# Performance work log

Measured on AMD Instinct MI355X. Metric: run time of the kernel, lower is better.

Reference implementation:

```python
import jax, jax.numpy as jnp
import numpy as np

B, C, H, W = 2, 512, 128, 128
L_NUM, HEADS, LEVELS, POINTS = 6, 8, 1, 4
HEAD_DIM = C // HEADS


def setup_inputs() -> dict:
    key = jax.random.key(0)
    ks = jax.random.split(key, 16)
    s = 0.02
    rn = lambda k, shape, scale=s: jax.random.normal(k, shape, jnp.float32) * scale
    return dict(
        bev_feat=jax.random.normal(ks[0], (B, C, H, W), jnp.float32),
        lidar_feat=jax.random.normal(ks[1], (B, C, H, W), jnp.float32),
        Wv=rn(ks[2], (L_NUM, C, C)), bv=jnp.zeros((L_NUM, C), jnp.float32),
        Woff=rn(ks[3], (L_NUM, C, HEADS * LEVELS * POINTS * 2)),
        boff=rn(ks[4], (L_NUM, HEADS * LEVELS * POINTS * 2), 0.5),
        Waw=rn(ks[5], (L_NUM, C, HEADS * LEVELS * POINTS)),
        baw=jnp.zeros((L_NUM, HEADS * LEVELS * POINTS), jnp.float32),
        Wout=rn(ks[6], (L_NUM, C, C)), bout=jnp.zeros((L_NUM, C), jnp.float32),
        ln1_g=jnp.ones((L_NUM, C), jnp.float32), ln1_b=jnp.zeros((L_NUM, C), jnp.float32),
        W1=rn(ks[7], (L_NUM, C, C)), W2=rn(ks[8], (L_NUM, C, C)),
        ln2_g=jnp.ones((L_NUM, C), jnp.float32), ln2_b=jnp.zeros((L_NUM, C), jnp.float32),
        pe_W1=rn(ks[9], (2, C), 0.5),
        pe_bn_g=jnp.ones((C,), jnp.float32), pe_bn_b=jnp.zeros((C,), jnp.float32),
        pe_bn_m=jnp.zeros((C,), jnp.float32), pe_bn_v=jnp.ones((C,), jnp.float32),
        pe_W2=rn(ks[10], (C, C)),
    )


def _layer_norm(x, g, b):
    mu = jnp.mean(x, -1, keepdims=True)
    var = jnp.mean((x - mu) ** 2, -1, keepdims=True)
    return (x - mu) * jax.lax.rsqrt(var + 1e-5) * g + b


def _bilinear_gather(v_flat, locx, locy):
    # v_flat: (B, heads, H*W, d); locx/locy: (B, heads, S) normalized [0,1]
    # grid_sample semantics: align_corners=False, zero padding
    x = locx * W - 0.5
    y = locy * H - 0.5
    x0f = jnp.floor(x); y0f = jnp.floor(y)
    wx = x - x0f; wy = y - y0f
    x0 = x0f.astype(jnp.int32); y0 = y0f.astype(jnp.int32)

    def corner(xi, yi, w):
        inb = (xi >= 0) & (xi < W) & (yi >= 0) & (yi < H)
        idx = jnp.clip(yi, 0, H - 1) * W + jnp.clip(xi, 0, W - 1)
        g = jnp.take_along_axis(v_flat, idx[..., None], axis=2)
        return g * (w * inb)[..., None]

    return (corner(x0, y0, (1 - wx) * (1 - wy)) + corner(x0 + 1, y0, wx * (1 - wy))
            + corner(x0, y0 + 1, (1 - wx) * wy) + corner(x0 + 1, y0 + 1, wx * wy))


def reference(bev_feat, lidar_feat, Wv, bv, Woff, boff, Waw, baw, Wout, bout,
              ln1_g, ln1_b, W1, W2, ln2_g, ln2_b,
              pe_W1, pe_bn_g, pe_bn_b, pe_bn_m, pe_bn_v, pe_W2):
    N = H * W
    # sparse voxelization: keep rows with all-nonzero features, pack valid-first per batch
    lf = jnp.transpose(lidar_feat, (0, 2, 3, 1)).reshape(B, N, C)
    mask = jnp.all(lf != 0, axis=-1)                       # (B,N)
    order = jnp.argsort((~mask).astype(jnp.int32), axis=1, stable=True)  # valid first
    valid = jnp.take_along_axis(mask, order, axis=1)       # (B,N)
    q = jnp.take_along_axis(lf, order[..., None], axis=1) * valid[..., None]
    hh = jnp.arange(N) // W
    ww = jnp.arange(N) % W
    ref_all = jnp.stack([ww / W, hh / H], -1).astype(jnp.float32)  # (N,2) = (x,y)
    ref = jnp.broadcast_to(ref_all, (B, N, 2))
    ref = jnp.take_along_axis(ref, order[..., None], axis=1) * valid[..., None]
    # learned positional embedding (BatchNorm in eval mode)
    pe = ref.reshape(B * N, 2) @ pe_W1
    pe = (pe - pe_bn_m) * jax.lax.rsqrt(pe_bn_v + 1e-5) * pe_bn_g + pe_bn_b
    q_pos = (jax.nn.relu(pe) @ pe_W2).reshape(B, N, C)
    feat_flat = jnp.transpose(bev_feat.reshape(B, C, N), (0, 2, 1))  # (B,N,C)
    norm_xy = jnp.array([W, H], jnp.float32)  # offset normalizer per level (w,h)
    for i in range(L_NUM):
        ident = q
        x = q + q_pos
        v = (feat_flat @ Wv[i] + bv[i]).reshape(B, N, HEADS, HEAD_DIM)
        v_flat = jnp.transpose(v, (0, 2, 1, 3))  # (B,heads,N,d)
        off = (x @ Woff[i] + boff[i]).reshape(B, N, HEADS, LEVELS * POINTS, 2)
        aw = jax.nn.softmax((x @ Waw[i] + baw[i]).reshape(B, N, HEADS, LEVELS * POINTS), axis=-1)
        loc = ref[:, :, None, None, :] + off / norm_xy      # (B,N,heads,P,2)
        locx = jnp.transpose(loc[..., 0], (0, 2, 1, 3)).reshape(B, HEADS, N * POINTS)
        locy = jnp.transpose(loc[..., 1], (0, 2, 1, 3)).reshape(B, HEADS, N * POINTS)
        samp = _bilinear_gather(v_flat, locx, locy).reshape(B, HEADS, N, POINTS, HEAD_DIM)
        awt = jnp.transpose(aw, (0, 2, 1, 3))               # (B,heads,N,P)
        out = jnp.sum(samp * awt[..., None], axis=3)        # (B,heads,N,d)
        out = jnp.transpose(out, (0, 2, 1, 3)).reshape(B, N, C)
        q = out @ Wout[i] + bout[i] + ident                 # dropout in eval = identity
        q = _layer_norm(q, ln1_g[i], ln1_b[i])
        q = jax.nn.relu(q @ W1[i]) @ W2[i] + q
        q = _layer_norm(q, ln2_g[i], ln2_b[i])
    # scatter back to dense (B,C,H,W); invalid voxels stay zero
    slots = jnp.zeros((B, N, C), q.dtype)
    slots = slots.at[jnp.arange(B)[:, None], order].set(q * valid[..., None])
    return jnp.transpose(slots.reshape(B, H, W, C), (0, 3, 1, 2))
```

## Files before the change

### kernel.cpp

```cpp
#include <hip/hip_runtime.h>
#include <cstdint>
#include <cstddef>

#define BDIM 2
#define CDIM 512
#define HDIM 128
#define WDIM 128
#define NDIM (HDIM * WDIM)
#define LNUM 6
#define NHEADS 8
#define HEAD_DIM 64
#define NPTS 4
#define BN_TOT (BDIM * NDIM)

typedef unsigned short u16;
typedef __attribute__((ext_vector_type(8))) short bf16x8;
typedef __attribute__((ext_vector_type(4))) float f32x4;

__device__ __forceinline__ u16 f2bf(float x) {
    unsigned u = __float_as_uint(x);
    u += 0x7fffu + ((u >> 16) & 1u);
    return (u16)(u >> 16);
}
__device__ __forceinline__ float bf2f(u16 h) {
    return __uint_as_float(((unsigned)h) << 16);
}

__device__ __forceinline__ void load_lds16(const void* g, void* l) {
    __builtin_amdgcn_global_load_lds(
        (const __attribute__((address_space(1))) void*)g,
        (__attribute__((address_space(3))) void*)l, 16, 0, 0);
}

__global__ void mask_kernel(const float* __restrict__ lidar, int* __restrict__ mask)
{
    int idx = blockIdx.x * blockDim.x + threadIdx.x;
    if (idx >= BN_TOT) return;
    int b = idx / NDIM;
    int n = idx - b * NDIM;
    const float* p = lidar + (size_t)b * CDIM * NDIM + n;
    int ok = 1;
#pragma unroll 8
    for (int c = 0; c < CDIM; ++c)
        ok &= (p[(size_t)c * NDIM] != 0.0f);
    mask[idx] = ok;
}

__global__ void order_kernel(const int* __restrict__ mask, int* __restrict__ order,
                             int* __restrict__ nvalid)
{
    int b = blockIdx.x;
    const int* m = mask + b * NDIM;
    int* ord = order + b * NDIM;
    __shared__ int part[256];
    __shared__ int totalValid;
    int t = threadIdx.x;
    const int CHUNK = NDIM / 256;
    int base = t * CHUNK;
    int cnt = 0;
    for (int i = 0; i < CHUNK; ++i) cnt += m[base + i];
    part[t] = cnt;
    __syncthreads();
    for (int s = 1; s < 256; s <<= 1) {
        int v = (t >= s) ? part[t - s] : 0;
        __syncthreads();
        part[t] += v;
        __syncthreads();
    }
    if (t == 255) { totalValid = part[255]; nvalid[b] = part[255]; }
    __syncthreads();
    int validBefore = (t == 0) ? 0 : part[t - 1];
    int nv = totalValid;
    for (int i = 0; i < CHUNK; ++i) {
        int n = base + i;
        if (m[n]) { ord[validBefore] = n; validBefore++; }
        else      { int invBefore = n - validBefore; ord[nv + invBefore] = n; }
    }
}

__global__ void ref_kernel(const int* __restrict__ order, const int* __restrict__ nvalid,
                           float* __restrict__ ref)
{
    int idx = blockIdx.x * blockDim.x + threadIdx.x;
    if (idx >= BN_TOT) return;
    int b = idx / NDIM;
    int j = idx - b * NDIM;
    int n = order[idx];
    float flag = (j < nvalid[b]) ? 1.0f : 0.0f;
    int hh = n / WDIM;
    int ww = n - hh * WDIM;
    ref[(size_t)idx * 2 + 0] = ((float)ww / (float)WDIM) * flag;
    ref[(size_t)idx * 2 + 1] = ((float)hh / (float)HDIM) * flag;
}

__global__ void pack_q_kernel(const float* __restrict__ lidar, const int* __restrict__ order,
                              const int* __restrict__ nvalid, u16* __restrict__ q)
{
    __shared__ float tile[32][33];
    __shared__ int ord_s[32];
    int b  = blockIdx.z;
    int j0 = blockIdx.x * 32;
    int c0 = blockIdx.y * 32;
    int tx = threadIdx.x, ty = threadIdx.y;
    if (ty == 0) ord_s[tx] = order[b * NDIM + j0 + tx];
    __syncthreads();
    const float* src = lidar + (size_t)b * CDIM * NDIM;
#pragma unroll
    for (int k = 0; k < 4; ++k) {
        int cl = ty * 4 + k;
        tile[cl][tx] = src[(size_t)(c0 + cl) * NDIM + ord_s[tx]];
    }
    __syncthreads();
    int nv = nvalid[b];
#pragma unroll
    for (int k = 0; k < 4; ++k) {
        int jl = ty * 4 + k;
        int j = j0 + jl;
        float f = (j < nv) ? 1.0f : 0.0f;
        q[((size_t)b * NDIM + j) * CDIM + c0 + tx] = f2bf(tile[tx][jl] * f);
    }
}

__global__ void scatter_kernel(const u16* __restrict__ q, const int* __restrict__ order,
                               const int* __restrict__ nvalid, float* __restrict__ out)
{
    __shared__ float tile[32][33];
    __shared__ int ord_s[32];
    int b  = blockIdx.z;
    int j0 = blockIdx.x * 32;
    int c0 = blockIdx.y * 32;
    int tx = threadIdx.x, ty = threadIdx.y;
    if (ty == 0) ord_s[tx] = order[b * NDIM + j0 + tx];
    __syncthreads();
    int nv = nvalid[b];
#pragma unroll
    for (int k = 0; k < 4; ++k) {
        int jl = ty * 4 + k;
        int j = j0 + jl;
        float f = (j < nv) ? 1.0f : 0.0f;
        tile[jl][tx] = bf2f(q[((size_t)b * NDIM + j) * CDIM + c0 + tx]) * f;
    }
    __syncthreads();
    float* dst = out + (size_t)b * CDIM * NDIM;
#pragma unroll
    for (int k = 0; k < 4; ++k) {
        int cl = ty * 4 + k;
        dst[(size_t)(c0 + cl) * NDIM + ord_s[tx]] = tile[tx][cl];
    }
}

__global__ void tconv_b_kernel(const float* __restrict__ src0, u16* __restrict__ dst0)
{
    __shared__ float t[32][33];
    int z = blockIdx.z;
    const float* src = src0 + (size_t)z * 512 * 512;
    u16* dst = dst0 + (size_t)z * 512 * 512;
    int k0 = blockIdx.x * 32, n0 = blockIdx.y * 32;
    int tx = threadIdx.x, ty = threadIdx.y;
#pragma unroll
    for (int j = 0; j < 4; ++j) {
        int kl = ty * 4 + j;
        t[kl][tx] = src[(size_t)(k0 + kl) * 512 + n0 + tx];
    }
    __syncthreads();
#pragma unroll
    for (int j = 0; j < 4; ++j) {
        int nl = ty * 4 + j;
        dst[(size_t)(n0 + nl) * 512 + k0 + tx] = f2bf(t[tx][nl]);
    }
}

__global__ void tconv_offaw_b_kernel(const float* __restrict__ woff0,
                                     const float* __restrict__ waw0,
                                     u16* __restrict__ dst0)
{
    __shared__ float t[32][33];
    int z = blockIdx.z;
    const float* woff = woff0 + (size_t)z * 512 * 64;
    const float* waw  = waw0 + (size_t)z * 512 * 32;
    u16* dst = dst0 + (size_t)z * 96 * 512;
    int k0 = blockIdx.x * 32, n0 = blockIdx.y * 32;
    int tx = threadIdx.x, ty = threadIdx.y;
#pragma unroll
    for (int j = 0; j < 4; ++j) {
        int kl = ty * 4 + j;
        int n = n0 + tx;
        float v = (n < 64) ? woff[(size_t)(k0 + kl) * 64 + n]
                           : waw[(size_t)(k0 + kl) * 32 + (n - 64)];
        t[kl][tx] = v;
    }
    __syncthreads();
#pragma unroll
    for (int j = 0; j < 4; ++j) {
        int nl = ty * 4 + j;
        dst[(size_t)(n0 + nl) * 512 + k0 + tx] = f2bf(t[tx][nl]);
    }
}

__global__ void bev_conv_kernel(const float* __restrict__ bev, u16* __restrict__ dst)
{
    __shared__ float t[32][33];
    int b  = blockIdx.z;
    int n0 = blockIdx.x * 32;
    int c0 = blockIdx.y * 32;
    int tx = threadIdx.x, ty = threadIdx.y;
    const float* src = bev + (size_t)b * CDIM * NDIM;
#pragma unroll
    for (int j = 0; j < 4; ++j) {
        int cl = ty * 4 + j;
        t[cl][tx] = src[(size_t)(c0 + cl) * NDIM + n0 + tx];
    }
    __syncthreads();
#pragma unroll
    for (int j = 0; j < 4; ++j) {
        int nl = ty * 4 + j;
        dst[((size_t)b * NDIM + n0 + nl) * CDIM + c0 + tx] = f2bf(t[tx][nl]);
    }
}

__global__ void pe_hidden_kernel(const float* __restrict__ ref, const float* __restrict__ W1,
                                 const float* __restrict__ g, const float* __restrict__ bb,
                                 const float* __restrict__ m, const float* __restrict__ v,
                                 u16* __restrict__ out)
{
    int row = blockIdx.x;
    float r0 = ref[(size_t)row * 2 + 0];
    float r1 = ref[(size_t)row * 2 + 1];
    for (int c = threadIdx.x; c < CDIM; c += blockDim.x) {
        float pe = r0 * W1[c] + r1 * W1[CDIM + c];
        pe = (pe - m[c]) * rsqrtf(v[c] + 1e-5f) * g[c] + bb[c];
        out[(size_t)row * CDIM + c] = f2bf(fmaxf(pe, 0.0f));
    }
}

__global__ void add_bf_kernel(const u16* __restrict__ q, const u16* __restrict__ qpos,
                              u16* __restrict__ x)
{
    size_t i = (size_t)blockIdx.x * blockDim.x + threadIdx.x;
    uint4 qa = ((const uint4*)q)[i];
    uint4 pv = ((const uint4*)qpos)[i];
    unsigned qw[4] = {qa.x, qa.y, qa.z, qa.w};
    unsigned pw[4] = {pv.x, pv.y, pv.z, pv.w};
    unsigned rw[4];
#pragma unroll
    for (int k = 0; k < 4; ++k) {
        float a0 = bf2f((u16)(qw[k] & 0xffff)), a1 = bf2f((u16)(qw[k] >> 16));
        float p0 = bf2f((u16)(pw[k] & 0xffff)), p1 = bf2f((u16)(pw[k] >> 16));
        rw[k] = (unsigned)f2bf(a0 + p0) | ((unsigned)f2bf(a1 + p1) << 16);
    }
    uint4 r; r.x = rw[0]; r.y = rw[1]; r.z = rw[2]; r.w = rw[3];
    ((uint4*)x)[i] = r;
}

__global__ __launch_bounds__(256) void gemm_bf16(
    const u16* __restrict__ A, const u16* __restrict__ Bt,
    const float* __restrict__ bias, u16* __restrict__ outB, int relu)
{
    __shared__ u16 As[2][128 * 32];
    __shared__ u16 Bs[2][128 * 32];
    int tid = threadIdx.x;
    int wave = tid >> 6, lane = tid & 63;
    int wr = wave >> 1, wc = wave & 1;
    int quad = lane >> 4, l15 = lane & 15;
    int bm = blockIdx.y * 128, bn = blockIdx.x * 128;

    f32x4 acc[4][4];
#pragma unroll
    for (int i = 0; i < 4; ++i)
#pragma unroll
        for (int j = 0; j < 4; ++j) { f32x4 z = {0.f, 0.f, 0.f, 0.f}; acc[i][j] = z; }

    int e0 = wave * 512 + lane * 8;
    int e1 = (wave + 4) * 512 + lane * 8;
    const u16* Ag0 = A + (size_t)(bm + (e0 >> 5)) * 512 + (e0 & 31);
    const u16* Ag1 = A + (size_t)(bm + (e1 >> 5)) * 512 + (e1 & 31);
    const u16* Bg0 = Bt + (size_t)(bn + (e0 >> 5)) * 512 + (e0 & 31);
    const u16* Bg1 = Bt + (size_t)(bn + (e1 >> 5)) * 512 + (e1 & 31);

    load_lds16(Ag0, &As[0][wave * 512]);
    load_lds16(Ag1, &As[0][(wave + 4) * 512]);
    load_lds16(Bg0, &Bs[0][wave * 512]);
    load_lds16(Bg1, &Bs[0][(wave + 4) * 512]);

    for (int it = 0; it < 16; ++it) {
        __syncthreads();
        int cur = it & 1, nxt = cur ^ 1;
        if (it < 15) {
            int kn = (it + 1) * 32;
            load_lds16(Ag0 + kn, &As[nxt][wave * 512]);
            load_lds16(Ag1 + kn, &As[nxt][(wave + 4) * 512]);
            load_lds16(Bg0 + kn, &Bs[nxt][wave * 512]);
            load_lds16(Bg1 + kn, &Bs[nxt][(wave + 4) * 512]);
        }
        bf16x8 av[4], bv[4];
#pragma unroll
        for (int mi = 0; mi < 4; ++mi)
            av[mi] = *(const bf16x8*)&As[cur][(wr * 64 + mi * 16 + l15) * 32 + quad * 8];
#pragma unroll
        for (int ni = 0; ni < 4; ++ni)
            bv[ni] = *(const bf16x8*)&Bs[cur][(wc * 64 + ni * 16 + l15) * 32 + quad * 8];
#pragma unroll
        for (int mi = 0; mi < 4; ++mi)
#pragma unroll
            for (int ni = 0; ni < 4; ++ni)
                acc[mi][ni] = __builtin_amdgcn_mfma_f32_16x16x32_bf16(
                    av[mi], bv[ni], acc[mi][ni], 0, 0, 0);
    }

    int rowb = bm + wr * 64;
    int colb = bn + wc * 64;
#pragma unroll
    for (int mi = 0; mi < 4; ++mi) {
#pragma unroll
        for (int ni = 0; ni < 4; ++ni) {
            int col = colb + ni * 16 + l15;
            float bi = bias ? bias[col] : 0.0f;
#pragma unroll
            for (int r = 0; r < 4; ++r) {
                int row = rowb + mi * 16 + quad * 4 + r;
                float val = acc[mi][ni][r] + bi;
                if (relu) val = fmaxf(val, 0.0f);
                outB[(size_t)row * 512 + col] = f2bf(val);
            }
        }
    }
}

__global__ __launch_bounds__(512, 4) void gemm_ln(
    const u16* __restrict__ A, const u16* __restrict__ Bt,
    const float* __restrict__ bias, const u16* __restrict__ resid,
    const float* __restrict__ g, const float* __restrict__ bta,
    u16* __restrict__ outQ, const u16* __restrict__ qpos, u16* __restrict__ outX)
{
    __shared__ u16 As[2][64 * 32];
    __shared__ u16 Bs[2][512 * 32];
    __shared__ float rs[8][64];
    __shared__ float rq[8][64];
    __shared__ float muL[64], invL[64];

    int tid = threadIdx.x;
    int wv = tid >> 6, lane = tid & 63;
    int quad = lane >> 4, l15 = lane & 15;
    int bm = blockIdx.x * 64;

    f32x4 acc[4][4];
#pragma unroll
    for (int i = 0; i < 4; ++i)
#pragma unroll
        for (int j = 0; j < 4; ++j) { f32x4 z = {0.f, 0.f, 0.f, 0.f}; acc[i][j] = z; }

    const u16* Ag = A + (size_t)(bm + wv * 16 + (lane >> 2)) * 512 + (lane & 3) * 8;
    const u16* Bg[4];
#pragma unroll
    for (int it = 0; it < 4; ++it) {
        int s = wv * 4 + it;
        Bg[it] = Bt + (size_t)(s * 16 + (lane >> 2)) * 512 + (lane & 3) * 8;
    }

    if (wv < 4) load_lds16(Ag, &As[0][wv * 512]);
#pragma unroll
    for (int it = 0; it < 4; ++it) load_lds16(Bg[it], &Bs[0][(wv * 4 + it) * 512]);

    for (int kk = 0; kk < 16; ++kk) {
        __syncthreads();
        int cur = kk & 1, nxt = cur ^ 1;
        if (kk < 15) {
            int kn = (kk + 1) * 32;
            if (wv < 4) load_lds16(Ag + kn, &As[nxt][wv * 512]);
#pragma unroll
            for (int it = 0; it < 4; ++it)
                load_lds16(Bg[it] + kn, &Bs[nxt][(wv * 4 + it) * 512]);
        }
        bf16x8 av[4], bv[4];
#pragma unroll
        for (int mi = 0; mi < 4; ++mi)
            av[mi] = *(const bf16x8*)&As[cur][(mi * 16 + l15) * 32 + quad * 8];
#pragma unroll
        for (int ni = 0; ni < 4; ++ni)
            bv[ni] = *(const bf16x8*)&Bs[cur][(wv * 64 + ni * 16 + l15) * 32 + quad * 8];
#pragma unroll
        for (int mi = 0; mi < 4; ++mi)
#pragma unroll
            for (int ni = 0; ni < 4; ++ni)
                acc[mi][ni] = __builtin_amdgcn_mfma_f32_16x16x32_bf16(
                    av[mi], bv[ni], acc[mi][ni], 0, 0, 0);
    }

    int colb = wv * 64;
    float biasv[4], gv[4], btv[4];
#pragma unroll
    for (int ni = 0; ni < 4; ++ni) {
        int c = colb + ni * 16 + l15;
        biasv[ni] = bias ? bias[c] : 0.0f;
        gv[ni] = g[c];
        btv[ni] = bta[c];
    }
#pragma unroll
    for (int mi = 0; mi < 4; ++mi) {
#pragma unroll
        for (int r = 0; r < 4; ++r) {
            size_t rowoff = (size_t)(bm + mi * 16 + quad * 4 + r) * 512;
#pragma unroll
            for (int ni = 0; ni < 4; ++ni) {
                int col = colb + ni * 16 + l15;
                acc[mi][ni][r] += biasv[ni] + bf2f(resid[rowoff + col]);
            }
        }
    }
#pragma unroll
    for (int mi = 0; mi < 4; ++mi) {
#pragma unroll
        for (int r = 0; r < 4; ++r) {
            float s = acc[mi][0][r] + acc[mi][1][r] + acc[mi][2][r] + acc[mi][3][r];
            float s2 = acc[mi][0][r] * acc[mi][0][r] + acc[mi][1][r] * acc[mi][1][r]
                     + acc[mi][2][r] * acc[mi][2][r] + acc[mi][3][r] * acc[mi][3][r];
#pragma unroll
            for (int m = 1; m < 16; m <<= 1) {
                s  += __shfl_xor(s, m, 64);
                s2 += __shfl_xor(s2, m, 64);
            }
            if (l15 == 0) {
                rs[wv][mi * 16 + quad * 4 + r] = s;
                rq[wv][mi * 16 + quad * 4 + r] = s2;
            }
        }
    }
    __syncthreads();
    if (tid < 64) {
        float s = 0.f, s2 = 0.f;
#pragma unroll
        for (int w = 0; w < 8; ++w) { s += rs[w][tid]; s2 += rq[w][tid]; }
        float mu = s * (1.0f / 512.0f);
        float var = s2 * (1.0f / 512.0f) - mu * mu;
        muL[tid] = mu;
        invL[tid] = rsqrtf(var + 1e-5f);
    }
    __syncthreads();
#pragma unroll
    for (int mi = 0; mi < 4; ++mi) {
#pragma unroll
        for (int r = 0; r < 4; ++r) {
            int lrow = mi * 16 + quad * 4 + r;
            float mu = muL[lrow], iv = invL[lrow];
            size_t rowoff = (size_t)(bm + lrow) * 512;
#pragma unroll
            for (int ni = 0; ni < 4; ++ni) {
                int col = colb + ni * 16 + l15;
                float y = (acc[mi][ni][r] - mu) * iv * gv[ni] + btv[ni];
                outQ[rowoff + col] = f2bf(y);
                if (outX)
                    outX[rowoff + col] = f2bf(y + bf2f(qpos[rowoff + col]));
            }
        }
    }
}

__global__ __launch_bounds__(256) void gemm_offaw(
    const u16* __restrict__ A, const u16* __restrict__ Bt,
    const float* __restrict__ boff, const float* __restrict__ baw,
    u16* __restrict__ offb, u16* __restrict__ awb)
{
    __shared__ u16 As[2][128 * 32];
    __shared__ u16 Bs[2][128 * 32];
    int tid = threadIdx.x;
    int wave = tid >> 6, lane = tid & 63;
    int wr = wave >> 1, wc = wave & 1;
    int quad = lane >> 4, l15 = lane & 15;
    int bm = blockIdx.y * 128;

    f32x4 acc[4][4];
#pragma unroll
    for (int i = 0; i < 4; ++i)
#pragma unroll
        for (int j = 0; j < 4; ++j) { f32x4 z = {0.f, 0.f, 0.f, 0.f}; acc[i][j] = z; }

    int e0 = wave * 512 + lane * 8;
    int e1 = (wave + 4) * 512 + lane * 8;
    int br0 = e0 >> 5; if (br0 > 95) br0 = 95;
    int br1 = e1 >> 5; if (br1 > 95) br1 = 95;
    const u16* Ag0 = A + (size_t)(bm + (e0 >> 5)) * 512 + (e0 & 31);
    const u16* Ag1 = A + (size_t)(bm + (e1 >> 5)) * 512 + (e1 & 31);
    const u16* Bg0 = Bt + (size_t)br0 * 512 + (e0 & 31);
    const u16* Bg1 = Bt + (size_t)br1 * 512 + (e1 & 31);

    load_lds16(Ag0, &As[0][wave * 512]);
    load_lds16(Ag1, &As[0][(wave + 4) * 512]);
    load_lds16(Bg0, &Bs[0][wave * 512]);
    load_lds16(Bg1, &Bs[0][(wave + 4) * 512]);

    for (int it = 0; it < 16; ++it) {
        __syncthreads();
        int cur = it & 1, nxt = cur ^ 1;
        if (it < 15) {
            int kn = (it + 1) * 32;
            load_lds16(Ag0 + kn, &As[nxt][wave * 512]);
            load_lds16(Ag1 + kn, &As[nxt][(wave + 4) * 512]);
            load_lds16(Bg0 + kn, &Bs[nxt][wave * 512]);
            load_lds16(Bg1 + kn, &Bs[nxt][(wave + 4) * 512]);
        }
        bf16x8 av[4], bv[4];
#pragma unroll
        for (int mi = 0; mi < 4; ++mi)
            av[mi] = *(const bf16x8*)&As[cur][(wr * 64 + mi * 16 + l15) * 32 + quad * 8];
#pragma unroll
        for (int ni = 0; ni < 4; ++ni)
            bv[ni] = *(const bf16x8*)&Bs[cur][(wc * 64 + ni * 16 + l15) * 32 + quad * 8];
#pragma unroll
        for (int mi = 0; mi < 4; ++mi)
#pragma unroll
            for (int ni = 0; ni < 4; ++ni)
                acc[mi][ni] = __builtin_amdgcn_mfma_f32_16x16x32_bf16(
                    av[mi], bv[ni], acc[mi][ni], 0, 0, 0);
    }

    int rowb = bm + wr * 64;
#pragma unroll
    for (int mi = 0; mi < 4; ++mi) {
#pragma unroll
        for (int ni = 0; ni < 4; ++ni) {
            int col = wc * 64 + ni * 16 + l15;
            if (col < 96) {
                float bi = (col < 64) ? boff[col] : baw[col - 64];
#pragma unroll
                for (int r = 0; r < 4; ++r) {
                    int row = rowb + mi * 16 + quad * 4 + r;
                    float val = acc[mi][ni][r] + bi;
                    if (col < 64) offb[(size_t)row * 64 + col] = f2bf(val);
                    else          awb[(size_t)row * 32 + (col - 64)] = f2bf(val);
                }
            }
        }
    }
}

__global__ __launch_bounds__(256) void sample_kernel(
    const float* __restrict__ ref, const u16* __restrict__ off,
    const u16* __restrict__ aw, const u16* __restrict__ v,
    u16* __restrict__ out)
{
    int bj = blockIdx.x * 4 + (threadIdx.x >> 6);
    int lane = threadIdx.x & 63;
    int h  = lane >> 3;
    int d8 = (lane & 7) * 8;
    int b  = bj >> 14;

    float rx = ref[(size_t)bj * 2 + 0];
    float ry = ref[(size_t)bj * 2 + 1];
    uint4 offv = *(const uint4*)(off + (size_t)bj * 64 + h * 8);
    uint2 awv  = *(const uint2*)(aw + (size_t)bj * 32 + h * 4);

    float l0 = bf2f((u16)(awv.x & 0xffff)), l1 = bf2f((u16)(awv.x >> 16));
    float l2 = bf2f((u16)(awv.y & 0xffff)), l3 = bf2f((u16)(awv.y >> 16));
    float mx = fmaxf(fmaxf(l0, l1), fmaxf(l2, l3));
    float e[4];
    e[0] = expf(l0 - mx); e[1] = expf(l1 - mx);
    e[2] = expf(l2 - mx); e[3] = expf(l3 - mx);
    float inv_es = 1.0f / (e[0] + e[1] + e[2] + e[3]);

    const u16* vb = v + (size_t)b * NDIM * CDIM + h * HEAD_DIM + d8;
    float acc[8] = {0.f, 0.f, 0.f, 0.f, 0.f, 0.f, 0.f, 0.f};
    unsigned ow[4] = {offv.x, offv.y, offv.z, offv.w};

#pragma unroll
    for (int p = 0; p < NPTS; ++p) {
        float ox = bf2f((u16)(ow[p] & 0xffff));
        float oy = bf2f((u16)(ow[p] >> 16));
        float X = rx * (float)WDIM + ox - 0.5f;
        float Y = ry * (float)HDIM + oy - 0.5f;
        float x0f = floorf(X), y0f = floorf(Y);
        float wx = X - x0f, wy = Y - y0f;
        int x0 = (int)x0f, y0 = (int)y0f;
        float ep = e[p];
#pragma unroll
        for (int cy = 0; cy < 2; ++cy) {
            int yy = y0 + cy;
            float wyc = cy ? wy : (1.0f - wy);
            int yin = (yy >= 0) & (yy < HDIM);
            int yc = min(max(yy, 0), HDIM - 1);
#pragma unroll
            for (int cx = 0; cx < 2; ++cx) {
                int xx = x0 + cx;
                float wxc = cx ? wx : (1.0f - wx);
                int xin = (xx >= 0) & (xx < WDIM);
                int xc = min(max(xx, 0), WDIM - 1);
                float wgt = ep * wyc * wxc * (float)(yin & xin);
                uint4 vv = *(const uint4*)(vb + (size_t)(yc * WDIM + xc) * CDIM);
                acc[0] += wgt * bf2f((u16)(vv.x & 0xffff));
                acc[1] += wgt * bf2f((u16)(vv.x >> 16));
                acc[2] += wgt * bf2f((u16)(vv.y & 0xffff));
                acc[3] += wgt * bf2f((u16)(vv.y >> 16));
                acc[4] += wgt * bf2f((u16)(vv.z & 0xffff));
                acc[5] += wgt * bf2f((u16)(vv.z >> 16));
                acc[6] += wgt * bf2f((u16)(vv.w & 0xffff));
                acc[7] += wgt * bf2f((u16)(vv.w >> 16));
            }
        }
    }
    uint4 r;
    r.x = (unsigned)f2bf(acc[0] * inv_es) | ((unsigned)f2bf(acc[1] * inv_es) << 16);
    r.y = (unsigned)f2bf(acc[2] * inv_es) | ((unsigned)f2bf(acc[3] * inv_es) << 16);
    r.z = (unsigned)f2bf(acc[4] * inv_es) | ((unsigned)f2bf(acc[5] * inv_es) << 16);
    r.w = (unsigned)f2bf(acc[6] * inv_es) | ((unsigned)f2bf(acc[7] * inv_es) << 16);
    *(uint4*)(out + (size_t)bj * CDIM + h * HEAD_DIM + d8) = r;
}

extern "C" void kernel_launch(void* const* d_in, const int* in_sizes, int n_in,
                              void* d_out, int out_size, void* d_ws, size_t ws_size,
                              hipStream_t stream)
{
    const float* bev   = (const float*)d_in[0];
    const float* lidar = (const float*)d_in[1];
    const float* Wv    = (const float*)d_in[2];
    const float* bv    = (const float*)d_in[3];
    const float* Woff  = (const float*)d_in[4];
    const float* boff  = (const float*)d_in[5];
    const float* Waw   = (const float*)d_in[6];
    const float* baw   = (const float*)d_in[7];
    const float* Wout  = (const float*)d_in[8];
    const float* bout  = (const float*)d_in[9];
    const float* ln1g  = (const float*)d_in[10];
    const float* ln1b  = (const float*)d_in[11];
    const float* W1    = (const float*)d_in[12];
    const float* W2    = (const float*)d_in[13];
    const float* ln2g  = (const float*)d_in[14];
    const float* ln2b  = (const float*)d_in[15];
    const float* peW1  = (const float*)d_in[16];
    const float* peg   = (const float*)d_in[17];
    const float* peb   = (const float*)d_in[18];
    const float* pem   = (const float*)d_in[19];
    const float* pev   = (const float*)d_in[20];
    const float* peW2  = (const float*)d_in[21];

    const size_t NC = (size_t)BN_TOT * CDIM;
    const size_t WSZ = 512 * 512;

    char* base = (char*)d_ws;
    u16* q      = (u16*)base;
    u16* actA   = (u16*)(base + NC * 2);
    u16* actB   = (u16*)(base + NC * 4);
    u16* wt     = (u16*)(base + NC * 6);
    u16* wtv    = wt;
    u16* wtout  = wt + 6 * WSZ;
    u16* wt1    = wt + 12 * WSZ;
    u16* wt2    = wt + 18 * WSZ;
    u16* wtpe   = wt + 24 * WSZ;
    u16* offawt = wt + 25 * WSZ;
    u16* offb   = offawt + 6 * 96 * 512;
    u16* awb    = offb + (size_t)BN_TOT * 64;
    float* refb = (float*)(awb + (size_t)BN_TOT * 32);
    int* mask   = (int*)(refb + (size_t)BN_TOT * 2);
    int* order  = mask + BN_TOT;
    int* nvalid = order + BN_TOT;

    u16* qpos_bf = (u16*)d_out;
    u16* featT   = (u16*)d_out + NC;

    dim3 blk328(32, 8);
    dim3 gemm_grid(4, 256);
    dim3 offaw_grid(1, 256);
    int  ln_grid = BN_TOT / 64;

    mask_kernel<<<BN_TOT / 256, 256, 0, stream>>>(lidar, mask);
    order_kernel<<<BDIM, 256, 0, stream>>>(mask, order, nvalid);
    ref_kernel<<<BN_TOT / 256, 256, 0, stream>>>(order, nvalid, refb);
    pack_q_kernel<<<dim3(NDIM / 32, CDIM / 32, BDIM), blk328, 0, stream>>>(lidar, order, nvalid, q);
    bev_conv_kernel<<<dim3(NDIM / 32, CDIM / 32, BDIM), blk328, 0, stream>>>(bev, featT);

    tconv_b_kernel<<<dim3(16, 16, 6), blk328, 0, stream>>>(Wv,   wtv);
    tconv_b_kernel<<<dim3(16, 16, 6), blk328, 0, stream>>>(Wout, wtout);
    tconv_b_kernel<<<dim3(16, 16, 6), blk328, 0, stream>>>(W1,   wt1);
    tconv_b_kernel<<<dim3(16, 16, 6), blk328, 0, stream>>>(W2,   wt2);
    tconv_b_kernel<<<dim3(16, 16, 1), blk328, 0, stream>>>(peW2, wtpe);
    tconv_offaw_b_kernel<<<dim3(16, 3, 6), blk328, 0, stream>>>(Woff, Waw, offawt);

    pe_hidden_kernel<<<BN_TOT, 128, 0, stream>>>(refb, peW1, peg, peb, pem, pev, actA);
    gemm_bf16<<<gemm_grid, 256, 0, stream>>>(actA, wtpe, nullptr, qpos_bf, 0);

    add_bf_kernel<<<(unsigned)(NC / 8 / 256), 256, 0, stream>>>(q, qpos_bf, actB);

    for (int i = 0; i < LNUM; ++i) {
        gemm_offaw<<<offaw_grid, 256, 0, stream>>>(actB, offawt + (size_t)i * 96 * 512,
                                                   boff + i * 64, baw + i * 32, offb, awb);
        gemm_bf16<<<gemm_grid, 256, 0, stream>>>(featT, wtv + (size_t)i * WSZ,
                                                 bv + i * CDIM, actA, 0);
        sample_kernel<<<BN_TOT / 4, 256, 0, stream>>>(refb, offb, awb, actA, actB);
        gemm_ln<<<ln_grid, 512, 0, stream>>>(actB, wtout + (size_t)i * WSZ, bout + i * CDIM,
                                             q, ln1g + i * CDIM, ln1b + i * CDIM,
                                             q, nullptr, nullptr);
        gemm_bf16<<<gemm_grid, 256, 0, stream>>>(q, wt1 + (size_t)i * WSZ, nullptr, actA, 1);
        gemm_ln<<<ln_grid, 512, 0, stream>>>(actA, wt2 + (size_t)i * WSZ, nullptr,
                                             q, ln2g + i * CDIM, ln2b + i * CDIM,
                                             q, qpos_bf,
                                             (i < LNUM - 1) ? actB : nullptr);
    }

    scatter_kernel<<<dim3(NDIM / 32, CDIM / 32, BDIM), blk328, 0, stream>>>(
        q, order, nvalid, (float*)d_out);
}
```

Measured before the change: 1.835 ms.

## Drop LDS staging in GEMMs, load MFMA fragments directly from global memory

All three GEMM kernels drop their double-buffered LDS staging and the per-iteration barriers. Each wave now loads its bf16 MFMA fragments straight from global memory with the K loop fully unrolled. The q+qpos add is moved into the offset/attention-weight GEMM's A-fragment load, which removes the separate add kernel and the extra outX write in the LayerNorm GEMM. This avoids LDS traffic and synchronisation, but operand tiles shared across waves are now fetched redundantly from global or L2 with small strided 16-byte loads, and gemm_ln loses its occupancy hint.

```diff
diff --git a/kernel.cpp b/kernel.cpp
--- a/kernel.cpp
+++ b/kernel.cpp
@@ -26,10 +26,23 @@
     return __uint_as_float(((unsigned)h) << 16);
 }
 
-__device__ __forceinline__ void load_lds16(const void* g, void* l) {
-    __builtin_amdgcn_global_load_lds(
-        (const __attribute__((address_space(1))) void*)g,
-        (__attribute__((address_space(3))) void*)l, 16, 0, 0);
+__device__ __forceinline__ bf16x8 ldfrag(const u16* p) {
+    return *(const bf16x8*)p;
+}
+
+__device__ __forceinline__ bf16x8 addpack(const u16* qp, const u16* pp) {
+    uint4 a = *(const uint4*)qp;
+    uint4 b = *(const uint4*)pp;
+    unsigned aw[4] = {a.x, a.y, a.z, a.w};
+    unsigned bw[4] = {b.x, b.y, b.z, b.w};
+    union { unsigned u[4]; bf16x8 h; } r;
+#pragma unroll
+    for (int k = 0; k < 4; ++k) {
+        float lo = bf2f((u16)(aw[k] & 0xffff)) + bf2f((u16)(bw[k] & 0xffff));
+        float hi = bf2f((u16)(aw[k] >> 16)) + bf2f((u16)(bw[k] >> 16));
+        r.u[k] = (unsigned)f2bf(lo) | ((unsigned)f2bf(hi) << 16);
+    }
+    return r.h;
 }
 
 __global__ void mask_kernel(const float* __restrict__ lidar, int* __restrict__ mask)
@@ -233,72 +246,39 @@
     }
 }
 
-__global__ void add_bf_kernel(const u16* __restrict__ q, const u16* __restrict__ qpos,
-                              u16* __restrict__ x)
-{
-    size_t i = (size_t)blockIdx.x * blockDim.x + threadIdx.x;
-    uint4 qa = ((const uint4*)q)[i];
-    uint4 pv = ((const uint4*)qpos)[i];
-    unsigned qw[4] = {qa.x, qa.y, qa.z, qa.w};
-    unsigned pw[4] = {pv.x, pv.y, pv.z, pv.w};
-    unsigned rw[4];
-#pragma unroll
-    for (int k = 0; k < 4; ++k) {
-        float a0 = bf2f((u16)(qw[k] & 0xffff)), a1 = bf2f((u16)(qw[k] >> 16));
-        float p0 = bf2f((u16)(pw[k] & 0xffff)), p1 = bf2f((u16)(pw[k] >> 16));
-        rw[k] = (unsigned)f2bf(a0 + p0) | ((unsigned)f2bf(a1 + p1) << 16);
-    }
-    uint4 r; r.x = rw[0]; r.y = rw[1]; r.z = rw[2]; r.w = rw[3];
-    ((uint4*)x)[i] = r;
-}
-
 __global__ __launch_bounds__(256) void gemm_bf16(
     const u16* __restrict__ A, const u16* __restrict__ Bt,
     const float* __restrict__ bias, u16* __restrict__ outB, int relu)
 {
-    __shared__ u16 As[2][128 * 32];
-    __shared__ u16 Bs[2][128 * 32];
     int tid = threadIdx.x;
-    int wave = tid >> 6, lane = tid & 63;
-    int wr = wave >> 1, wc = wave & 1;
+    int wv = tid >> 6, lane = tid & 63;
+    int wr = wv >> 1, wc = wv & 1;
     int quad = lane >> 4, l15 = lane & 15;
     int bm = blockIdx.y * 128, bn = blockIdx.x * 128;
 
+    const u16* Ap[4];
+    const u16* Bp[4];
+#pragma unroll
+    for (int mi = 0; mi < 4; ++mi)
+        Ap[mi] = A + (size_t)(bm + wr * 64 + mi * 16 + l15) * 512 + quad * 8;
+#pragma unroll
+    for (int ni = 0; ni < 4; ++ni)
+        Bp[ni] = Bt + (size_t)(bn + wc * 64 + ni * 16 + l15) * 512 + quad * 8;
+
     f32x4 acc[4][4];
 #pragma unroll
     for (int i = 0; i < 4; ++i)
 #pragma unroll
         for (int j = 0; j < 4; ++j) { f32x4 z = {0.f, 0.f, 0.f, 0.f}; acc[i][j] = z; }
 
-    int e0 = wave * 512 + lane * 8;
-    int e1 = (wave + 4) * 512 + lane * 8;
-    const u16* Ag0 = A + (size_t)(bm + (e0 >> 5)) * 512 + (e0 & 31);
-    const u16* Ag1 = A + (size_t)(bm + (e1 >> 5)) * 512 + (e1 & 31);
-    const u16* Bg0 = Bt + (size_t)(bn + (e0 >> 5)) * 512 + (e0 & 31);
-    const u16* Bg1 = Bt + (size_t)(bn + (e1 >> 5)) * 512 + (e1 & 31);
-
-    load_lds16(Ag0, &As[0][wave * 512]);
-    load_lds16(Ag1, &As[0][(wave + 4) * 512]);
-    load_lds16(Bg0, &Bs[0][wave * 512]);
-    load_lds16(Bg1, &Bs[0][(wave + 4) * 512]);
-
+#pragma unroll
     for (int it = 0; it < 16; ++it) {
-        __syncthreads();
-        int cur = it & 1, nxt = cur ^ 1;
-        if (it < 15) {
-            int kn = (it + 1) * 32;
-            load_lds16(Ag0 + kn, &As[nxt][wave * 512]);
-            load_lds16(Ag1 + kn, &As[nxt][(wave + 4) * 512]);
-            load_lds16(Bg0 + kn, &Bs[nxt][wave * 512]);
-            load_lds16(Bg1 + kn, &Bs[nxt][(wave + 4) * 512]);
-        }
+        int k0 = it * 32;
         bf16x8 av[4], bv[4];
 #pragma unroll
-        for (int mi = 0; mi < 4; ++mi)
-            av[mi] = *(const bf16x8*)&As[cur][(wr * 64 + mi * 16 + l15) * 32 + quad * 8];
-#pragma unroll
-        for (int ni = 0; ni < 4; ++ni)
-            bv[ni] = *(const bf16x8*)&Bs[cur][(wc * 64 + ni * 16 + l15) * 32 + quad * 8];
+        for (int mi = 0; mi < 4; ++mi) av[mi] = ldfrag(Ap[mi] + k0);
+#pragma unroll
+        for (int ni = 0; ni < 4; ++ni) bv[ni] = ldfrag(Bp[ni] + k0);
 #pragma unroll
         for (int mi = 0; mi < 4; ++mi)
 #pragma unroll
@@ -326,14 +306,12 @@
     }
 }
 
-__global__ __launch_bounds__(512, 4) void gemm_ln(
+__global__ __launch_bounds__(512) void gemm_ln(
     const u16* __restrict__ A, const u16* __restrict__ Bt,
     const float* __restrict__ bias, const u16* __restrict__ resid,
     const float* __restrict__ g, const float* __restrict__ bta,
-    u16* __restrict__ outQ, const u16* __restrict__ qpos, u16* __restrict__ outX)
-{
-    __shared__ u16 As[2][64 * 32];
-    __shared__ u16 Bs[2][512 * 32];
+    u16* __restrict__ outQ)
+{
     __shared__ float rs[8][64];
     __shared__ float rq[8][64];
     __shared__ float muL[64], invL[64];
@@ -343,41 +321,29 @@
     int quad = lane >> 4, l15 = lane & 15;
     int bm = blockIdx.x * 64;
 
+    const u16* Ap[4];
+    const u16* Bp[4];
+#pragma unroll
+    for (int mi = 0; mi < 4; ++mi)
+        Ap[mi] = A + (size_t)(bm + mi * 16 + l15) * 512 + quad * 8;
+#pragma unroll
+    for (int ni = 0; ni < 4; ++ni)
+        Bp[ni] = Bt + (size_t)(wv * 64 + ni * 16 + l15) * 512 + quad * 8;
+
     f32x4 acc[4][4];
 #pragma unroll
     for (int i = 0; i < 4; ++i)
 #pragma unroll
         for (int j = 0; j < 4; ++j) { f32x4 z = {0.f, 0.f, 0.f, 0.f}; acc[i][j] = z; }
 
-    const u16* Ag = A + (size_t)(bm + wv * 16 + (lane >> 2)) * 512 + (lane & 3) * 8;
-    const u16* Bg[4];
-#pragma unroll
-    for (int it = 0; it < 4; ++it) {
-        int s = wv * 4 + it;
-        Bg[it] = Bt + (size_t)(s * 16 + (lane >> 2)) * 512 + (lane & 3) * 8;
-    }
-
-    if (wv < 4) load_lds16(Ag, &As[0][wv * 512]);
-#pragma unroll
-    for (int it = 0; it < 4; ++it) load_lds16(Bg[it], &Bs[0][(wv * 4 + it) * 512]);
-
-    for (int kk = 0; kk < 16; ++kk) {
-        __syncthreads();
-        int cur = kk & 1, nxt = cur ^ 1;
-        if (kk < 15) {
-            int kn = (kk + 1) * 32;
-            if (wv < 4) load_lds16(Ag + kn, &As[nxt][wv * 512]);
-#pragma unroll
-            for (int it = 0; it < 4; ++it)
-                load_lds16(Bg[it] + kn, &Bs[nxt][(wv * 4 + it) * 512]);
-        }
+#pragma unroll
+    for (int it = 0; it < 16; ++it) {
+        int k0 = it * 32;
         bf16x8 av[4], bv[4];
 #pragma unroll
-        for (int mi = 0; mi < 4; ++mi)
-            av[mi] = *(const bf16x8*)&As[cur][(mi * 16 + l15) * 32 + quad * 8];
-#pragma unroll
-        for (int ni = 0; ni < 4; ++ni)
-            bv[ni] = *(const bf16x8*)&Bs[cur][(wv * 64 + ni * 16 + l15) * 32 + quad * 8];
+        for (int mi = 0; mi < 4; ++mi) av[mi] = ldfrag(Ap[mi] + k0);
+#pragma unroll
+        for (int ni = 0; ni < 4; ++ni) bv[ni] = ldfrag(Bp[ni] + k0);
 #pragma unroll
         for (int mi = 0; mi < 4; ++mi)
 #pragma unroll
@@ -448,63 +414,53 @@
                 int col = colb + ni * 16 + l15;
                 float y = (acc[mi][ni][r] - mu) * iv * gv[ni] + btv[ni];
                 outQ[rowoff + col] = f2bf(y);
-                if (outX)
-                    outX[rowoff + col] = f2bf(y + bf2f(qpos[rowoff + col]));
             }
         }
     }
 }
 
 __global__ __launch_bounds__(256) void gemm_offaw(
-    const u16* __restrict__ A, const u16* __restrict__ Bt,
+    const u16* __restrict__ q, const u16* __restrict__ qpos,
+    const u16* __restrict__ Bt,
     const float* __restrict__ boff, const float* __restrict__ baw,
     u16* __restrict__ offb, u16* __restrict__ awb)
 {
-    __shared__ u16 As[2][128 * 32];
-    __shared__ u16 Bs[2][128 * 32];
     int tid = threadIdx.x;
-    int wave = tid >> 6, lane = tid & 63;
-    int wr = wave >> 1, wc = wave & 1;
+    int wv = tid >> 6, lane = tid & 63;
+    int wr = wv & 1, wc = wv >> 1;
     int quad = lane >> 4, l15 = lane & 15;
     int bm = blockIdx.y * 128;
 
+    const u16* Qp[4];
+    const u16* Pp[4];
+    const u16* Bp[4];
+#pragma unroll
+    for (int mi = 0; mi < 4; ++mi) {
+        size_t off = (size_t)(bm + wr * 64 + mi * 16 + l15) * 512 + quad * 8;
+        Qp[mi] = q + off;
+        Pp[mi] = qpos + off;
+    }
+#pragma unroll
+    for (int ni = 0; ni < 4; ++ni) {
+        int brow = wc * 64 + ni * 16 + l15;
+        if (brow > 95) brow = 95;
+        Bp[ni] = Bt + (size_t)brow * 512 + quad * 8;
+    }
+
     f32x4 acc[4][4];
 #pragma unroll
     for (int i = 0; i < 4; ++i)
 #pragma unroll
         for (int j = 0; j < 4; ++j) { f32x4 z = {0.f, 0.f, 0.f, 0.f}; acc[i][j] = z; }
 
-    int e0 = wave * 512 + lane * 8;
-    int e1 = (wave + 4) * 512 + lane * 8;
-    int br0 = e0 >> 5; if (br0 > 95) br0 = 95;
-    int br1 = e1 >> 5; if (br1 > 95) br1 = 95;
-    const u16* Ag0 = A + (size_t)(bm + (e0 >> 5)) * 512 + (e0 & 31);
-    const u16* Ag1 = A + (size_t)(bm + (e1 >> 5)) * 512 + (e1 & 31);
-    const u16* Bg0 = Bt + (size_t)br0 * 512 + (e0 & 31);
-    const u16* Bg1 = Bt + (size_t)br1 * 512 + (e1 & 31);
-
-    load_lds16(Ag0, &As[0][wave * 512]);
-    load_lds16(Ag1, &As[0][(wave + 4) * 512]);
-    load_lds16(Bg0, &Bs[0][wave * 512]);
-    load_lds16(Bg1, &Bs[0][(wave + 4) * 512]);
-
+#pragma unroll
     for (int it = 0; it < 16; ++it) {
-        __syncthreads();
-        int cur = it & 1, nxt = cur ^ 1;
-        if (it < 15) {
-            int kn = (it + 1) * 32;
-            load_lds16(Ag0 + kn, &As[nxt][wave * 512]);
-            load_lds16(Ag1 + kn, &As[nxt][(wave + 4) * 512]);
-            load_lds16(Bg0 + kn, &Bs[nxt][wave * 512]);
-            load_lds16(Bg1 + kn, &Bs[nxt][(wave + 4) * 512]);
-        }
+        int k0 = it * 32;
         bf16x8 av[4], bv[4];
 #pragma unroll
-        for (int mi = 0; mi < 4; ++mi)
-            av[mi] = *(const bf16x8*)&As[cur][(wr * 64 + mi * 16 + l15) * 32 + quad * 8];
-#pragma unroll
-        for (int ni = 0; ni < 4; ++ni)
-            bv[ni] = *(const bf16x8*)&Bs[cur][(wc * 64 + ni * 16 + l15) * 32 + quad * 8];
+        for (int mi = 0; mi < 4; ++mi) av[mi] = addpack(Qp[mi] + k0, Pp[mi] + k0);
+#pragma unroll
+        for (int ni = 0; ni < 4; ++ni) bv[ni] = ldfrag(Bp[ni] + k0);
 #pragma unroll
         for (int mi = 0; mi < 4; ++mi)
 #pragma unroll
@@ -676,22 +632,18 @@
     pe_hidden_kernel<<<BN_TOT, 128, 0, stream>>>(refb, peW1, peg, peb, pem, pev, actA);
     gemm_bf16<<<gemm_grid, 256, 0, stream>>>(actA, wtpe, nullptr, qpos_bf, 0);
 
-    add_bf_kernel<<<(unsigned)(NC / 8 / 256), 256, 0, stream>>>(q, qpos_bf, actB);
-
     for (int i = 0; i < LNUM; ++i) {
-        gemm_offaw<<<offaw_grid, 256, 0, stream>>>(actB, offawt + (size_t)i * 96 * 512,
+        gemm_offaw<<<offaw_grid, 256, 0, stream>>>(q, qpos_bf,
+                                                   offawt + (size_t)i * 96 * 512,
                                                    boff + i * 64, baw + i * 32, offb, awb);
         gemm_bf16<<<gemm_grid, 256, 0, stream>>>(featT, wtv + (size_t)i * WSZ,
                                                  bv + i * CDIM, actA, 0);
         sample_kernel<<<BN_TOT / 4, 256, 0, stream>>>(refb, offb, awb, actA, actB);
         gemm_ln<<<ln_grid, 512, 0, stream>>>(actB, wtout + (size_t)i * WSZ, bout + i * CDIM,
-                                             q, ln1g + i * CDIM, ln1b + i * CDIM,
-                                             q, nullptr, nullptr);
+                                             q, ln1g + i * CDIM, ln1b + i * CDIM, q);
         gemm_bf16<<<gemm_grid, 256, 0, stream>>>(q, wt1 + (size_t)i * WSZ, nullptr, actA, 1);
         gemm_ln<<<ln_grid, 512, 0, stream>>>(actA, wt2 + (size_t)i * WSZ, nullptr,
-                                             q, ln2g + i * CDIM, ln2b + i * CDIM,
-                                             q, qpos_bf,
-                                             (i < LNUM - 1) ? actB : nullptr);
+                                             q, ln2g + i * CDIM, ln2b + i * CDIM, q);
     }
 
     scatter_kernel<<<dim3(NDIM / 32, CDIM / 32, BDIM), blk328, 0, stream>>>(
```

Result: slower. 2.398 ms (+30.7%).
